# Optimization experiments

Hardware: AMD Instinct MI355X
Metric: run time of the kernel (lower is better)

## Reference

```python
import jax, jax.numpy as jnp
import numpy as np

TEMPERATURE = 0.5


def setup_inputs() -> dict:
    key = jax.random.key(0)
    k1, k2 = jax.random.split(key)
    N, D = 4096, 256
    z_i = jax.random.normal(k1, (N, D), dtype=jnp.float32)
    z_j = jax.random.normal(k2, (N, D), dtype=jnp.float32)
    return {"z_i": z_i, "z_j": z_j}


def reference(z_i, z_j):
    N = z_i.shape[0]
    z = jnp.concatenate([z_i, z_j], axis=0)            # (2N, D)
    sim = (z @ z.T) / TEMPERATURE                       # (2N, 2N)
    # mask self-similarity on the diagonal
    diag = jnp.eye(2 * N, dtype=bool)
    sim = jnp.where(diag, -jnp.inf, sim)
    # positive pair labels: i <-> i+N
    labels = jnp.concatenate([jnp.arange(N, 2 * N), jnp.arange(0, N)])
    logp = jax.nn.log_softmax(sim, axis=-1)             # (2N, 2N)
    loss = -jnp.mean(jnp.take_along_axis(logp, labels[:, None], axis=-1))
    return loss
```

## Files before the change

### kernel.cpp

```cpp
#include <hip/hip_runtime.h>
#include <hip/hip_bf16.h>


typedef __bf16 bf16x8 __attribute__((ext_vector_type(8)));
typedef __bf16 bf16x4 __attribute__((ext_vector_type(4)));
typedef float  f32x4  __attribute__((ext_vector_type(4)));

#define NPAIR 4096
#define NROW  8192
#define DIM   256
#define NCHUNK 128
#define SQSCALE 1.6986437f
#define LN2F    0.6931471805599453f
#define M2      176.0f

#define EXP2F(x) __builtin_amdgcn_exp2f(x)

__global__ __launch_bounds__(256) void k_convert(const float* __restrict__ zi,
                                                 const float* __restrict__ zj,
                                                 __bf16* __restrict__ Zp,
                                                 float* __restrict__ pos,
                                                 float* __restrict__ out) {
    const int w = threadIdx.x >> 6, lane = threadIdx.x & 63;
    const int r = blockIdx.x * 4 + w;
    if (blockIdx.x == 0 && threadIdx.x == 0) out[0] = 0.0f;
    const float4 vi = *(const float4*)(zi + r * DIM + lane * 4);
    const float4 vj = *(const float4*)(zj + r * DIM + lane * 4);
    bf16x4 bi, bj;
    bi[0] = (__bf16)(vi.x * SQSCALE); bi[1] = (__bf16)(vi.y * SQSCALE);
    bi[2] = (__bf16)(vi.z * SQSCALE); bi[3] = (__bf16)(vi.w * SQSCALE);
    bj[0] = (__bf16)(vj.x * SQSCALE); bj[1] = (__bf16)(vj.y * SQSCALE);
    bj[2] = (__bf16)(vj.z * SQSCALE); bj[3] = (__bf16)(vj.w * SQSCALE);
    char* Zb = (char*)Zp;
    *(bf16x4*)(Zb + (size_t)r * 512 + lane * 8) = bi;
    *(bf16x4*)(Zb + (size_t)(r + NPAIR) * 512 + lane * 8) = bj;
    float d = vi.x * vj.x + vi.y * vj.y + vi.z * vj.z + vi.w * vj.w;
    #pragma unroll
    for (int m = 32; m >= 1; m >>= 1) d += __shfl_xor(d, m);
    if (lane == 0) pos[r] = 2.0f * d;
}

__global__ __launch_bounds__(512, 2) void k_lse(const __bf16* __restrict__ Zp,
                                                float* __restrict__ Lpart) {
    const int bid = blockIdx.x;
    const int br = bid >> 5, bc = bid & 31;
    const int tid = threadIdx.x;
    const int w = tid >> 6, lane = tid & 63;
    const int wr = w >> 2, wc = w & 3;
    const int l15 = lane & 15, l4 = lane >> 4;

    __shared__ __align__(16) char smem[65536];
    const char* Zb = (const char*)Zp;
    const int arow0 = br * 256, brow0 = bc * 256;

    const int j16sw = (l4 * 16) ^ ((lane & 3) << 4);
    const int aBase = (wr * 128 + l15) * 64 + j16sw;
    const int bBase = (wc * 64  + l15) * 64 + j16sw;

    #define STAGE(KT) do {                                                           \
        char* db = smem + ((KT) & 1) * 32768;                                        \
        _Pragma("unroll")                                                            \
        for (int q = 0; q < 2; q++) {                                                \
            const int c = q * 512 + tid;                                             \
            const int row = c >> 2;                                                  \
            const int inner = ((c & 3) * 16) ^ ((row & 3) << 4);                     \
            __builtin_amdgcn_global_load_lds(                                        \
                (const __attribute__((address_space(1))) unsigned int*)              \
                    (Zb + (size_t)(arow0 + row) * 512 + (KT) * 64 + inner),          \
                (__attribute__((address_space(3))) unsigned int*)(db + c * 16),      \
                16, 0, 0);                                                           \
        }                                                                            \
        _Pragma("unroll")                                                            \
        for (int q = 0; q < 2; q++) {                                                \
            const int c = q * 512 + tid;                                             \
            const int row = c >> 2;                                                  \
            const int inner = ((c & 3) * 16) ^ ((row & 3) << 4);                     \
            __builtin_amdgcn_global_load_lds(                                        \
                (const __attribute__((address_space(1))) unsigned int*)              \
                    (Zb + (size_t)(brow0 + row) * 512 + (KT) * 64 + inner),          \
                (__attribute__((address_space(3))) unsigned int*)(db + 16384 + c * 16), \
                16, 0, 0);                                                           \
        }                                                                            \
    } while (0)

    #define DECL(M) f32x4 c##M##0 = (f32x4)(0.0f), c##M##1 = (f32x4)(0.0f), \
                          c##M##2 = (f32x4)(0.0f), c##M##3 = (f32x4)(0.0f);
    DECL(0) DECL(1) DECL(2) DECL(3) DECL(4) DECL(5) DECL(6) DECL(7)
    #undef DECL

    STAGE(0);
    STAGE(1);

    #define MROW(M, AF) \
        c##M##0 = __builtin_amdgcn_mfma_f32_16x16x32_bf16(AF, b0, c##M##0, 0, 0, 0); \
        c##M##1 = __builtin_amdgcn_mfma_f32_16x16x32_bf16(AF, b1, c##M##1, 0, 0, 0); \
        c##M##2 = __builtin_amdgcn_mfma_f32_16x16x32_bf16(AF, b2, c##M##2, 0, 0, 0); \
        c##M##3 = __builtin_amdgcn_mfma_f32_16x16x32_bf16(AF, b3, c##M##3, 0, 0, 0);

    for (int kt = 0; kt < 8; ++kt) {
        if (kt < 7) { asm volatile("s_waitcnt vmcnt(4)" ::: "memory"); }
        else        { asm volatile("s_waitcnt vmcnt(0)" ::: "memory"); }
        __builtin_amdgcn_s_barrier();
        const char* Ab = smem + (kt & 1) * 32768;
        const char* Bb = Ab + 16384;
        bf16x8 a0 = *(const bf16x8*)(Ab + aBase + 0 * 1024);
        bf16x8 a1 = *(const bf16x8*)(Ab + aBase + 1 * 1024);
        bf16x8 a2 = *(const bf16x8*)(Ab + aBase + 2 * 1024);
        bf16x8 a3 = *(const bf16x8*)(Ab + aBase + 3 * 1024);
        bf16x8 a4 = *(const bf16x8*)(Ab + aBase + 4 * 1024);
        bf16x8 a5 = *(const bf16x8*)(Ab + aBase + 5 * 1024);
        bf16x8 a6 = *(const bf16x8*)(Ab + aBase + 6 * 1024);
        bf16x8 a7 = *(const bf16x8*)(Ab + aBase + 7 * 1024);
        bf16x8 b0 = *(const bf16x8*)(Bb + bBase + 0 * 1024);
        bf16x8 b1 = *(const bf16x8*)(Bb + bBase + 1 * 1024);
        bf16x8 b2 = *(const bf16x8*)(Bb + bBase + 2 * 1024);
        bf16x8 b3 = *(const bf16x8*)(Bb + bBase + 3 * 1024);
        __builtin_amdgcn_s_setprio(1);
        MROW(0, a0) MROW(1, a1) MROW(2, a2) MROW(3, a3)
        MROW(4, a4) MROW(5, a5) MROW(6, a6) MROW(7, a7)
        __builtin_amdgcn_s_setprio(0);
        __builtin_amdgcn_s_barrier();
        if (kt < 6) STAGE(kt + 2);
    }
    #undef MROW
    #undef STAGE

    const bool diagblk = (br == bc);
    const bool dlane = (l15 >> 2) == l4;
    const int dreg = lane & 3;
    float* Lp = Lpart + (size_t)(bc * 4 + wc) * NROW + arow0 + wr * 128;

    #define EPIT(MT, NT) {                                                           \
        f32x4 v = c##MT##NT;                                                         \
        const bool dp = diagblk && dlane && (wr * 128 + (MT) * 16 == wc * 64 + (NT) * 16); \
        r0 += EXP2F(((dp && dreg == 0) ? -1e30f : v[0]) - M2);                       \
        r1 += EXP2F(((dp && dreg == 1) ? -1e30f : v[1]) - M2);                       \
        r2 += EXP2F(((dp && dreg == 2) ? -1e30f : v[2]) - M2);                       \
        r3 += EXP2F(((dp && dreg == 3) ? -1e30f : v[3]) - M2);                       \
    }
    #define EPI(MT) {                                                                \
        float r0 = 0.0f, r1 = 0.0f, r2 = 0.0f, r3 = 0.0f;                            \
        EPIT(MT, 0) EPIT(MT, 1) EPIT(MT, 2) EPIT(MT, 3)                              \
        r0 += __shfl_xor(r0, 1); r0 += __shfl_xor(r0, 2);                            \
        r0 += __shfl_xor(r0, 4); r0 += __shfl_xor(r0, 8);                            \
        r1 += __shfl_xor(r1, 1); r1 += __shfl_xor(r1, 2);                            \
        r1 += __shfl_xor(r1, 4); r1 += __shfl_xor(r1, 8);                            \
        r2 += __shfl_xor(r2, 1); r2 += __shfl_xor(r2, 2);                            \
        r2 += __shfl_xor(r2, 4); r2 += __shfl_xor(r2, 8);                            \
        r3 += __shfl_xor(r3, 1); r3 += __shfl_xor(r3, 2);                            \
        r3 += __shfl_xor(r3, 4); r3 += __shfl_xor(r3, 8);                            \
        if (l15 == 0) *(float4*)(Lp + (MT) * 16 + l4 * 4) = make_float4(r0, r1, r2, r3); \
    }
    EPI(0) EPI(1) EPI(2) EPI(3) EPI(4) EPI(5) EPI(6) EPI(7)
    #undef EPI
    #undef EPIT
}

__global__ __launch_bounds__(256) void k_final(const float* __restrict__ Lpart,
                                               const float* __restrict__ pos,
                                               float* __restrict__ out) {
    __shared__ float red[256];
    const int t = threadIdx.x;
    const int r = blockIdx.x * 256 + t;
    float l = 0.0f;
    #pragma unroll 8
    for (int s = 0; s < NCHUNK; s++) l += Lpart[(size_t)s * NROW + r];
    const float lse = (M2 + __builtin_log2f(l)) * LN2F;
    red[t] = lse - pos[r & (NPAIR - 1)];
    __syncthreads();
    for (int ofs = 128; ofs > 0; ofs >>= 1) {
        if (t < ofs) red[t] += red[t + ofs];
        __syncthreads();
    }
    if (t == 0) atomicAdd(out, red[0] / (float)NROW);
}

extern "C" void kernel_launch(void* const* d_in, const int* in_sizes, int n_in,
                              void* d_out, int out_size, void* d_ws, size_t ws_size,
                              hipStream_t stream) {
    const float* zi = (const float*)d_in[0];
    const float* zj = (const float*)d_in[1];
    __bf16* Zp   = (__bf16*)d_ws;
    float* pos   = (float*)((char*)d_ws + (size_t)NROW * DIM * 2);
    float* Lpart = pos + NPAIR;

    k_convert<<<NPAIR / 4, 256, 0, stream>>>(zi, zj, Zp, pos, (float*)d_out);
    k_lse<<<32 * 32, 512, 0, stream>>>(Zp, Lpart);
    k_final<<<NROW / 256, 256, 0, stream>>>(Lpart, pos, (float*)d_out);
}
```

Before: 113.9 us.

## Software-pipeline LDS fragment loads across k-tiles and change LDS swizzle pattern

Unrolls the k-loop and splits each tile's MFMA work into two halves. The next tile's A and B fragments are loaded from LDS in the middle of the current tile's math, using ping-pong B register sets. This hides LDS read latency behind MFMAs and places the refill stage issue earlier. The XOR swizzle also changes to key off bits of the chunk index rather than row&3, aimed at fewer LDS bank conflicts. The trade-offs are higher register pressure and an extra barrier per tile.

```diff
diff --git a/kernel.cpp b/kernel.cpp
--- a/kernel.cpp
+++ b/kernel.cpp
@@ -53,7 +53,7 @@
     const char* Zb = (const char*)Zp;
     const int arow0 = br * 256, brow0 = bc * 256;
 
-    const int j16sw = (l4 * 16) ^ ((lane & 3) << 4);
+    const int j16sw = (l4 * 16) ^ (((l15 >> 1) & 3) << 4);
     const int aBase = (wr * 128 + l15) * 64 + j16sw;
     const int bBase = (wc * 64  + l15) * 64 + j16sw;
 
@@ -63,7 +63,7 @@
         for (int q = 0; q < 2; q++) {                                                \
             const int c = q * 512 + tid;                                             \
             const int row = c >> 2;                                                  \
-            const int inner = ((c & 3) * 16) ^ ((row & 3) << 4);                     \
+            const int inner = ((c & 3) * 16) ^ (((c >> 3) & 3) << 4);                \
             __builtin_amdgcn_global_load_lds(                                        \
                 (const __attribute__((address_space(1))) unsigned int*)              \
                     (Zb + (size_t)(arow0 + row) * 512 + (KT) * 64 + inner),          \
@@ -74,7 +74,7 @@
         for (int q = 0; q < 2; q++) {                                                \
             const int c = q * 512 + tid;                                             \
             const int row = c >> 2;                                                  \
-            const int inner = ((c & 3) * 16) ^ ((row & 3) << 4);                     \
+            const int inner = ((c & 3) * 16) ^ (((c >> 3) & 3) << 4);                \
             __builtin_amdgcn_global_load_lds(                                        \
                 (const __attribute__((address_space(1))) unsigned int*)              \
                     (Zb + (size_t)(brow0 + row) * 512 + (KT) * 64 + inner),          \
@@ -88,40 +88,72 @@
     DECL(0) DECL(1) DECL(2) DECL(3) DECL(4) DECL(5) DECL(6) DECL(7)
     #undef DECL
 
+    bf16x8 a0, a1, a2, a3, a4, a5, a6, a7;
+    bf16x8 bP0, bP1, bP2, bP3, bQ0, bQ1, bQ2, bQ3;
+
+    #define MROW(M, AF, BS) \
+        c##M##0 = __builtin_amdgcn_mfma_f32_16x16x32_bf16(AF, b##BS##0, c##M##0, 0, 0, 0); \
+        c##M##1 = __builtin_amdgcn_mfma_f32_16x16x32_bf16(AF, b##BS##1, c##M##1, 0, 0, 0); \
+        c##M##2 = __builtin_amdgcn_mfma_f32_16x16x32_bf16(AF, b##BS##2, c##M##2, 0, 0, 0); \
+        c##M##3 = __builtin_amdgcn_mfma_f32_16x16x32_bf16(AF, b##BS##3, c##M##3, 0, 0, 0);
+
     STAGE(0);
     STAGE(1);
-
-    #define MROW(M, AF) \
-        c##M##0 = __builtin_amdgcn_mfma_f32_16x16x32_bf16(AF, b0, c##M##0, 0, 0, 0); \
-        c##M##1 = __builtin_amdgcn_mfma_f32_16x16x32_bf16(AF, b1, c##M##1, 0, 0, 0); \
-        c##M##2 = __builtin_amdgcn_mfma_f32_16x16x32_bf16(AF, b2, c##M##2, 0, 0, 0); \
-        c##M##3 = __builtin_amdgcn_mfma_f32_16x16x32_bf16(AF, b3, c##M##3, 0, 0, 0);
-
-    for (int kt = 0; kt < 8; ++kt) {
-        if (kt < 7) { asm volatile("s_waitcnt vmcnt(4)" ::: "memory"); }
-        else        { asm volatile("s_waitcnt vmcnt(0)" ::: "memory"); }
-        __builtin_amdgcn_s_barrier();
-        const char* Ab = smem + (kt & 1) * 32768;
+    asm volatile("s_waitcnt vmcnt(4)" ::: "memory");
+    __builtin_amdgcn_s_barrier();
+    {
+        const char* Ab = smem;
         const char* Bb = Ab + 16384;
-        bf16x8 a0 = *(const bf16x8*)(Ab + aBase + 0 * 1024);
-        bf16x8 a1 = *(const bf16x8*)(Ab + aBase + 1 * 1024);
-        bf16x8 a2 = *(const bf16x8*)(Ab + aBase + 2 * 1024);
-        bf16x8 a3 = *(const bf16x8*)(Ab + aBase + 3 * 1024);
-        bf16x8 a4 = *(const bf16x8*)(Ab + aBase + 4 * 1024);
-        bf16x8 a5 = *(const bf16x8*)(Ab + aBase + 5 * 1024);
-        bf16x8 a6 = *(const bf16x8*)(Ab + aBase + 6 * 1024);
-        bf16x8 a7 = *(const bf16x8*)(Ab + aBase + 7 * 1024);
-        bf16x8 b0 = *(const bf16x8*)(Bb + bBase + 0 * 1024);
-        bf16x8 b1 = *(const bf16x8*)(Bb + bBase + 1 * 1024);
-        bf16x8 b2 = *(const bf16x8*)(Bb + bBase + 2 * 1024);
-        bf16x8 b3 = *(const bf16x8*)(Bb + bBase + 3 * 1024);
-        __builtin_amdgcn_s_setprio(1);
-        MROW(0, a0) MROW(1, a1) MROW(2, a2) MROW(3, a3)
-        MROW(4, a4) MROW(5, a5) MROW(6, a6) MROW(7, a7)
-        __builtin_amdgcn_s_setprio(0);
-        __builtin_amdgcn_s_barrier();
-        if (kt < 6) STAGE(kt + 2);
-    }
+        a0 = *(const bf16x8*)(Ab + aBase + 0 * 1024);
+        a1 = *(const bf16x8*)(Ab + aBase + 1 * 1024);
+        a2 = *(const bf16x8*)(Ab + aBase + 2 * 1024);
+        a3 = *(const bf16x8*)(Ab + aBase + 3 * 1024);
+        bP0 = *(const bf16x8*)(Bb + bBase + 0 * 1024);
+        bP1 = *(const bf16x8*)(Bb + bBase + 1 * 1024);
+        bP2 = *(const bf16x8*)(Bb + bBase + 2 * 1024);
+        bP3 = *(const bf16x8*)(Bb + bBase + 3 * 1024);
+    }
+
+    #define KTBODY(KT, BC, BN, WS) {                                                 \
+        const char* Ab = smem + ((KT) & 1) * 32768;                                  \
+        a4 = *(const bf16x8*)(Ab + aBase + 4 * 1024);                                \
+        a5 = *(const bf16x8*)(Ab + aBase + 5 * 1024);                                \
+        a6 = *(const bf16x8*)(Ab + aBase + 6 * 1024);                                \
+        a7 = *(const bf16x8*)(Ab + aBase + 7 * 1024);                                \
+        __builtin_amdgcn_s_setprio(1);                                               \
+        MROW(0, a0, BC) MROW(1, a1, BC) MROW(2, a2, BC) MROW(3, a3, BC)              \
+        __builtin_amdgcn_s_setprio(0);                                               \
+        asm volatile("s_waitcnt lgkmcnt(0)" ::: "memory");         \
+        __builtin_amdgcn_s_barrier();                                                \
+        if ((KT) < 6) STAGE((KT) + 2);                                               \
+        if ((KT) < 7) {                                                              \
+            asm volatile("s_waitcnt vmcnt(" WS ")" ::: "memory");                    \
+            __builtin_amdgcn_s_barrier();                                            \
+            const char* Ab2 = smem + (((KT) + 1) & 1) * 32768;                       \
+            const char* Bb2 = Ab2 + 16384;                                           \
+            a0 = *(const bf16x8*)(Ab2 + aBase + 0 * 1024);                           \
+            a1 = *(const bf16x8*)(Ab2 + aBase + 1 * 1024);                           \
+            a2 = *(const bf16x8*)(Ab2 + aBase + 2 * 1024);                           \
+            a3 = *(const bf16x8*)(Ab2 + aBase + 3 * 1024);                           \
+            b##BN##0 = *(const bf16x8*)(Bb2 + bBase + 0 * 1024);                     \
+            b##BN##1 = *(const bf16x8*)(Bb2 + bBase + 1 * 1024);                     \
+            b##BN##2 = *(const bf16x8*)(Bb2 + bBase + 2 * 1024);                     \
+            b##BN##3 = *(const bf16x8*)(Bb2 + bBase + 3 * 1024);                     \
+        }                                                                            \
+        __builtin_amdgcn_s_setprio(1);                                               \
+        MROW(4, a4, BC) MROW(5, a5, BC) MROW(6, a6, BC) MROW(7, a7, BC)              \
+        __builtin_amdgcn_s_setprio(0);                                               \
+    }
+
+    KTBODY(0, P, Q, "4")
+    KTBODY(1, Q, P, "4")
+    KTBODY(2, P, Q, "4")
+    KTBODY(3, Q, P, "4")
+    KTBODY(4, P, Q, "4")
+    KTBODY(5, Q, P, "4")
+    KTBODY(6, P, Q, "0")
+    KTBODY(7, Q, P, "0")
+    #undef KTBODY
     #undef MROW
     #undef STAGE
 
```

Measured after the change: 111.1 us. 1.02x faster.
